# Kernel tuning notes

Measured on AMD Instinct MI355X. Metric: run time of the kernel, lower is better.

The kernel has to match this reference:

```python
import jax, jax.numpy as jnp
import numpy as np

BS, SEQ, D, H = 2, 2048, 1024, 16
HD = D // H  # head_dim = 64


def setup_inputs() -> dict:
    key = jax.random.key(0)
    kx, kw = jax.random.split(key)
    x = jax.random.normal(kx, (BS, SEQ, D), dtype=jnp.float32)
    # qkv Linear: weight [3D, D] (xavier_normal), bias zeros
    std = float(np.sqrt(2.0 / (D + 3 * D)))
    W_qkv = jax.random.normal(kw, (3 * D, D), dtype=jnp.float32) * std
    b_qkv = jnp.zeros((3 * D,), dtype=jnp.float32)
    return {"x": x, "W_qkv": W_qkv, "b_qkv": b_qkv}


def reference(x, W_qkv, b_qkv):
    bs, seq_len, embed_dim = x.shape
    # fused QKV projection: [bs, seq, 3D]
    qkv = x @ W_qkv.T + b_qkv
    qkv = qkv.reshape(bs, seq_len, 3, H, HD)
    qkv = jnp.transpose(qkv, (2, 0, 3, 1, 4))  # [3, bs, H, seq, HD]
    Q, K, V = qkv[0], qkv[1], qkv[2]
    # past_kv is None -> total_len == seq_len, past_len == 0
    scores = jnp.einsum("bhqd,bhkd->bhqk", Q, K) / jnp.sqrt(jnp.float32(HD))
    # causal mask: True above diagonal -> -inf
    mask = jnp.triu(jnp.ones((seq_len, seq_len), dtype=bool), k=1)
    scores = jnp.where(mask[None, None, :, :], -jnp.inf, scores)
    probs = jax.nn.softmax(scores, axis=-1)
    # attn_dropout = 0.0 (eval) -> identity
    out = jnp.einsum("bhqk,bhkd->bhqd", probs, V)
    out = jnp.transpose(out, (0, 2, 1, 3)).reshape(bs, seq_len, embed_dim)
    return (out, (K, V))
```

## Files before the change

kernel.cpp:

```cpp
#include <hip/hip_runtime.h>

typedef __bf16 bf16_t;
typedef __bf16 bf16x8 __attribute__((ext_vector_type(8)));
typedef float f32x4 __attribute__((ext_vector_type(4)));
typedef unsigned long long u64;

__device__ __forceinline__ unsigned short bfbits(float f) {
  unsigned u = __float_as_uint(f);
  u += 0x7fffu + ((u >> 16) & 1u);
  return (unsigned short)(u >> 16);
}
__device__ __forceinline__ bf16_t f2bf(float f) {
  unsigned short s = bfbits(f);
  union { unsigned short s; bf16_t b; } cv; cv.s = s; return cv.b;
}

__device__ __forceinline__ void gl16(const void* g, void* l) {
  __builtin_amdgcn_global_load_lds(
      (const __attribute__((address_space(1))) void*)g,
      (__attribute__((address_space(3))) void*)l,
      16, 0, 0);
}

__global__ __launch_bounds__(256) void cvt_kernel(const float* __restrict__ x,
                                                  const float* __restrict__ Wf,
                                                  bf16_t* __restrict__ xb,
                                                  bf16_t* __restrict__ wb) {
  const int i = blockIdx.x * 256 + threadIdx.x;
  const float* src; bf16_t* dst; int j;
  if (i < 524288) { j = i; src = x; dst = xb; }
  else            { j = i - 524288; src = Wf; dst = wb; }
  const float4* s = (const float4*)src + (size_t)j * 2;
  float4 a = s[0], b = s[1];
  bf16x8 o;
  o[0] = f2bf(a.x); o[1] = f2bf(a.y); o[2] = f2bf(a.z); o[3] = f2bf(a.w);
  o[4] = f2bf(b.x); o[5] = f2bf(b.y); o[6] = f2bf(b.z); o[7] = f2bf(b.w);
  const int row = j >> 7, jr = j & 127;
  const int dstc = (row << 7) + (jr & ~3) + ((jr & 3) ^ ((row >> 1) & 3));
  *((bf16x8*)dst + dstc) = o;
}

#define GEMM_K 1024
__global__ __launch_bounds__(256) void qkv_gemm(
    const bf16_t* __restrict__ A,
    const bf16_t* __restrict__ B,
    const float* __restrict__ bias,
    float* __restrict__ Ko, float* __restrict__ Vo,
    bf16_t* __restrict__ Qb, bf16_t* __restrict__ Kb,
    bf16_t* __restrict__ Vt,
    int* __restrict__ qcnt)
{
  if (blockIdx.x == 0 && threadIdx.x == 0) *qcnt = 0;
  __shared__ bf16_t lsA[3][4096];
  __shared__ bf16_t lsB[3][4096];
  const int tid = threadIdx.x;
  const int lane = tid & 63;
  const int ln = lane & 15, qd = lane >> 4;
  const int wid = tid >> 6;
  const int wm = wid & 1, wn = wid >> 1;
  const int xcd = blockIdx.x & 7;
  const int j = blockIdx.x >> 3;
  const int bn = xcd * 3 + (j % 3);
  const int bm = j / 3;
  const int m0 = bm * 128, n0 = bn * 128;
  const int qs = qd ^ ((ln >> 1) & 3);

  f32x4 acc[4][4] = {};

  const int c0 = tid, c1 = tid + 256;
  const bf16_t* ga0 = A + (size_t)(m0 + (c0 >> 2)) * GEMM_K + (c0 & 3) * 8;
  const bf16_t* ga1 = A + (size_t)(m0 + (c1 >> 2)) * GEMM_K + (c1 & 3) * 8;
  const bf16_t* gb0 = B + (size_t)(n0 + (c0 >> 2)) * GEMM_K + (c0 & 3) * 8;
  const bf16_t* gb1 = B + (size_t)(n0 + (c1 >> 2)) * GEMM_K + (c1 & 3) * 8;

#define STAGE(t, slot)                                   \
  do {                                                   \
    const int ko_ = (t) * 32;                            \
    gl16(ga0 + ko_, &lsA[(slot)][c0 * 8]);               \
    gl16(ga1 + ko_, &lsA[(slot)][c1 * 8]);               \
    gl16(gb0 + ko_, &lsB[(slot)][c0 * 8]);               \
    gl16(gb1 + ko_, &lsB[(slot)][c1 * 8]);               \
  } while (0)

#define COMPUTE(slot)                                                          \
  do {                                                                         \
    bf16x8 af[4], bf[4];                                                       \
    _Pragma("unroll")                                                          \
    for (int mi = 0; mi < 4; ++mi)                                             \
      af[mi] = *(const bf16x8*)&lsA[(slot)][(wm * 64 + mi * 16 + ln) * 32 + qs * 8]; \
    _Pragma("unroll")                                                          \
    for (int ni = 0; ni < 4; ++ni)                                             \
      bf[ni] = *(const bf16x8*)&lsB[(slot)][(wn * 64 + ni * 16 + ln) * 32 + qs * 8]; \
    _Pragma("unroll")                                                          \
    for (int mi = 0; mi < 4; ++mi)                                             \
      _Pragma("unroll")                                                        \
      for (int ni = 0; ni < 4; ++ni)                                           \
        acc[mi][ni] = __builtin_amdgcn_mfma_f32_16x16x32_bf16(af[mi], bf[ni], acc[mi][ni], 0, 0, 0); \
  } while (0)

#define WAITBAR(n)                                        \
  do {                                                    \
    asm volatile("s_waitcnt vmcnt(" #n ")" ::: "memory"); \
    __builtin_amdgcn_s_barrier();                         \
  } while (0)

  STAGE(0, 0);
  STAGE(1, 1);
#pragma unroll
  for (int t = 0; t < 30; ++t) {
    WAITBAR(4);
    STAGE(t + 2, (t + 2) % 3);
    COMPUTE(t % 3);
  }
  WAITBAR(4); COMPUTE(0);
  WAITBAR(0); COMPUTE(1);

#undef STAGE
#undef COMPUTE
#undef WAITBAR

  const int sec = n0 >> 10;
#pragma unroll
  for (int mi = 0; mi < 4; ++mi) {
#pragma unroll
    for (int ni = 0; ni < 4; ++ni) {
      const int colg = n0 + wn * 64 + ni * 16 + ln;
      const float bv = bias[colg];
      const int cc = colg & 1023, h = cc >> 6, hd = cc & 63;
      if (sec == 2) {
        unsigned u[4];
#pragma unroll
        for (int r = 0; r < 4; ++r) {
          const int mg = m0 + wm * 64 + mi * 16 + qd * 4 + r;
          const int b = mg >> 11, s = mg & 2047;
          const float val = acc[mi][ni][r] + bv;
          Vo[((size_t)((b * 16 + h) * 2048 + s)) * 64 + hd] = val;
          u[r] = __float_as_uint(val);
        }
        const int mg0 = m0 + wm * 64 + mi * 16 + qd * 4;
        const int b0 = mg0 >> 11, s0 = mg0 & 2047;
        const unsigned lo = (u[1] & 0xFFFF0000u) | (u[0] >> 16);
        const unsigned hi = (u[3] & 0xFFFF0000u) | (u[2] >> 16);
        const size_t vb = (size_t)(b0 * 16 + h) * 131072 + (size_t)(s0 >> 6) * 4096 +
                          (size_t)hd * 64 + ((((s0 >> 3) & 7) ^ (hd & 7)) << 3) + (s0 & 7);
        *(u64*)&Vt[vb] = ((u64)hi << 32) | lo;
      } else {
#pragma unroll
        for (int r = 0; r < 4; ++r) {
          const int mg = m0 + wm * 64 + mi * 16 + qd * 4 + r;
          const int b = mg >> 11, s = mg & 2047;
          const float val = acc[mi][ni][r] + bv;
          const int bhi = b * 16 + h;
          const size_t sidx = (size_t)bhi * 131072 + (size_t)(s >> 6) * 4096 +
                              (size_t)(s & 63) * 64 + (((hd >> 3) ^ (s & 7)) << 3) + (hd & 7);
          if (sec == 0) {
            Qb[sidx] = f2bf(val * 0.18033688f);
          } else {
            Ko[((size_t)(bhi * 2048 + s)) * 64 + hd] = val;
            Kb[sidx] = f2bf(val);
          }
        }
      }
    }
  }
}

__global__ __launch_bounds__(512, 4) void attn_kernel(
    const bf16_t* __restrict__ Qb,
    const bf16_t* __restrict__ Kb,
    const bf16_t* __restrict__ Vt,
    float* __restrict__ Out,
    int* __restrict__ qcnt)
{
  __shared__ bf16_t lk[8192];
  __shared__ bf16_t lv[8192];
  __shared__ bf16_t lp[8192];
  __shared__ int task_sh;
  const int tid = threadIdx.x;
  const int lane = tid & 63, ln = lane & 15, qd = lane >> 4;
  const int w = tid >> 6;
  const int l7 = ln & 7;

  for (;;) {
    __syncthreads();
    if (tid == 0) task_sh = atomicAdd(qcnt, 1);
    __syncthreads();
    const int task = task_sh;
    if (task >= 512) break;
    const int it = (task < 256) ? (15 - (task >> 5)) : ((task - 256) >> 5);
    const int bh = task & 31;
    const int b = bh >> 4, h = bh & 15;

    const bf16_t* qbase = Qb + (size_t)bh * 131072 + (size_t)it * 8192;
    const bf16_t* kbase = Kb + (size_t)bh * 131072;
    const bf16_t* vbase = Vt + (size_t)bh * 131072;

#pragma unroll
    for (int i = 0; i < 2; ++i) {
      const int cc = tid + i * 512;
      gl16(kbase + cc * 8, &lk[cc * 8]);
      gl16(vbase + cc * 8, &lv[cc * 8]);
    }

    bf16x8 afq[2];
    {
      const int row = w * 16 + ln;
#pragma unroll
      for (int kk = 0; kk < 2; ++kk)
        afq[kk] = *(const bf16x8*)(qbase + (row >> 6) * 4096 + (row & 63) * 64 +
                                   (((kk * 4 + qd) ^ l7) << 3));
    }
    __syncthreads();

    f32x4 oc[4] = {};
    float lsum = 0.f;
    const int qg = it * 128 + w * 16 + ln;
    const int q = w * 16 + ln;

    for (int st = 0; st <= it; ++st) {
      if (st > 0) {
        __syncthreads();
#pragma unroll
        for (int i = 0; i < 2; ++i) {
          const int cc = tid + i * 512;
          gl16(kbase + (size_t)st * 8192 + cc * 8, &lk[cc * 8]);
          gl16(vbase + (size_t)st * 8192 + cc * 8, &lv[cc * 8]);
        }
        __syncthreads();
      }
      const bool diag = (st == it);

#pragma unroll
      for (int h2 = 0; h2 < 2; ++h2) {
        const int lofs = h2 * 4096;
        f32x4 sa[4] = {};
#pragma unroll
        for (int kk = 0; kk < 2; ++kk) {
          bf16x8 ak[4];
#pragma unroll
          for (int ki = 0; ki < 4; ++ki)
            ak[ki] = *(const bf16x8*)&lk[lofs + (ki * 16 + ln) * 64 + (((kk * 4 + qd) ^ l7) << 3)];
#pragma unroll
          for (int ki = 0; ki < 4; ++ki)
            sa[ki] = __builtin_amdgcn_mfma_f32_16x16x32_bf16(ak[ki], afq[kk], sa[ki], 0, 0, 0);
        }

#pragma unroll
        for (int ki = 0; ki < 4; ++ki) {
          const int kb0 = (st * 2 + h2) * 64 + ki * 16 + qd * 4;
          float p0 = __builtin_amdgcn_exp2f(sa[ki][0]);
          float p1 = __builtin_amdgcn_exp2f(sa[ki][1]);
          float p2 = __builtin_amdgcn_exp2f(sa[ki][2]);
          float p3 = __builtin_amdgcn_exp2f(sa[ki][3]);
          if (diag) {
            if (kb0 + 0 > qg) p0 = 0.f;
            if (kb0 + 1 > qg) p1 = 0.f;
            if (kb0 + 2 > qg) p2 = 0.f;
            if (kb0 + 3 > qg) p3 = 0.f;
          }
          lsum += (p0 + p1) + (p2 + p3);
          const unsigned lo = (__float_as_uint(p1) & 0xFFFF0000u) | (__float_as_uint(p0) >> 16);
          const unsigned hi = (__float_as_uint(p3) & 0xFFFF0000u) | (__float_as_uint(p2) >> 16);
          const int g = (ki * 2 + (qd >> 1)) ^ l7;
          *(u64*)&lp[q * 64 + g * 8 + (qd & 1) * 4] = ((u64)hi << 32) | lo;
        }

#pragma unroll
        for (int kk = 0; kk < 2; ++kk) {
          bf16x8 afp, bfv[4];
          afp = *(const bf16x8*)&lp[q * 64 + (((kk * 4 + qd) ^ l7) << 3)];
#pragma unroll
          for (int ni = 0; ni < 4; ++ni)
            bfv[ni] = *(const bf16x8*)&lv[lofs + (ni * 16 + ln) * 64 + (((kk * 4 + qd) ^ l7) << 3)];
#pragma unroll
          for (int ni = 0; ni < 4; ++ni)
            oc[ni] = __builtin_amdgcn_mfma_f32_16x16x32_bf16(afp, bfv[ni], oc[ni], 0, 0, 0);
        }
      }
    }

    float ls = lsum;
    ls += __shfl_xor(ls, 16);
    ls += __shfl_xor(ls, 32);
#pragma unroll
    for (int r = 0; r < 4; ++r) {
      const float lval = __shfl(ls, qd * 4 + r);
      const float inv = 1.0f / lval;
      const int rowq = it * 128 + w * 16 + qd * 4 + r;
#pragma unroll
      for (int ni = 0; ni < 4; ++ni) {
        const int colh = ni * 16 + ln;
        Out[(size_t)(b * 2048 + rowq) * 1024 + h * 64 + colh] = oc[ni][r] * inv;
      }
    }
  }
}

extern "C" void kernel_launch(void* const* d_in, const int* in_sizes, int n_in,
                              void* d_out, int out_size, void* d_ws, size_t ws_size,
                              hipStream_t stream) {
  const float* x = (const float*)d_in[0];
  const float* W = (const float*)d_in[1];
  const float* bq = (const float*)d_in[2];
  float* out = (float*)d_out;
  float* Ko = out + 4194304;
  float* Vo = out + 8388608;
  char* ws = (char*)d_ws;
  bf16_t* xb = (bf16_t*)ws;
  bf16_t* wb = (bf16_t*)(ws + 8388608);
  bf16_t* Qb = (bf16_t*)(ws + 14680064);
  bf16_t* Kb = (bf16_t*)(ws + 23068672);
  bf16_t* Vt = (bf16_t*)(ws + 31457280);
  int*    qcnt = (int*)(ws + 39845888);

  hipLaunchKernelGGL(cvt_kernel, dim3(3584), dim3(256), 0, stream, x, W, xb, wb);
  hipLaunchKernelGGL(qkv_gemm, dim3(768), dim3(256), 0, stream, xb, wb, bq, Ko, Vo, Qb, Kb, Vt, qcnt);
  hipLaunchKernelGGL(attn_kernel, dim3(512), dim3(512), 0, stream, Qb, Kb, Vt, out, qcnt);
}
```

Measured before the change: 161.5 us.

## Double-buffer K/V tiles in LDS and skip fully masked diagonal subtile

Splits the K/V shared-memory staging into two 64-key slots and prefetches the next tile with async global-to-LDS loads while computing the current one. The two __syncthreads per 128-key block become a vmcnt wait plus barrier per 64-key tile. Waves whose query rows all lie before the final 64-key tile now skip it, since it is entirely masked. The risk is that the single wait-and-barrier must also cover the reuse of the P scratch buffer and the overwrite of the slot just read.

```diff
diff --git a/kernel.cpp b/kernel.cpp
--- a/kernel.cpp
+++ b/kernel.cpp
@@ -172,8 +172,8 @@
     float* __restrict__ Out,
     int* __restrict__ qcnt)
 {
-  __shared__ bf16_t lk[8192];
-  __shared__ bf16_t lv[8192];
+  __shared__ bf16_t lk[2][4096];
+  __shared__ bf16_t lv[2][4096];
   __shared__ bf16_t lp[8192];
   __shared__ int task_sh;
   const int tid = threadIdx.x;
@@ -195,13 +195,73 @@
     const bf16_t* kbase = Kb + (size_t)bh * 131072;
     const bf16_t* vbase = Vt + (size_t)bh * 131072;
 
-#pragma unroll
-    for (int i = 0; i < 2; ++i) {
-      const int cc = tid + i * 512;
-      gl16(kbase + cc * 8, &lk[cc * 8]);
-      gl16(vbase + cc * 8, &lv[cc * 8]);
-    }
-
+    f32x4 oc[4] = {};
+    float lsum = 0.f;
+    const int qg = it * 128 + w * 16 + ln;
+    const int q = w * 16 + ln;
+    const int nt = 2 * (it + 1);
+
+#define STG(t, slot)                                              \
+    do {                                                          \
+      gl16(kbase + (size_t)(t) * 4096 + tid * 8, &lk[(slot)][tid * 8]); \
+      gl16(vbase + (size_t)(t) * 4096 + tid * 8, &lv[(slot)][tid * 8]); \
+    } while (0)
+
+#define CTILE(kt, slot)                                                        \
+    do {                                                                       \
+      if (!((kt) == 2 * it + 1 && w < 4)) {                                    \
+        const bool diag = ((kt) >= 2 * it);                                    \
+        f32x4 sa[4] = {};                                                      \
+        _Pragma("unroll")                                                      \
+        for (int kk = 0; kk < 2; ++kk) {                                       \
+          bf16x8 ak[4];                                                        \
+          _Pragma("unroll")                                                    \
+          for (int ki = 0; ki < 4; ++ki)                                       \
+            ak[ki] = *(const bf16x8*)&lk[(slot)][(ki * 16 + ln) * 64 + (((kk * 4 + qd) ^ l7) << 3)]; \
+          _Pragma("unroll")                                                    \
+          for (int ki = 0; ki < 4; ++ki)                                       \
+            sa[ki] = __builtin_amdgcn_mfma_f32_16x16x32_bf16(ak[ki], afq[kk], sa[ki], 0, 0, 0); \
+        }                                                                      \
+        _Pragma("unroll")                                                      \
+        for (int ki = 0; ki < 4; ++ki) {                                       \
+          const int kb0 = (kt) * 64 + ki * 16 + qd * 4;                        \
+          float p0 = __builtin_amdgcn_exp2f(sa[ki][0]);                        \
+          float p1 = __builtin_amdgcn_exp2f(sa[ki][1]);                        \
+          float p2 = __builtin_amdgcn_exp2f(sa[ki][2]);                        \
+          float p3 = __builtin_amdgcn_exp2f(sa[ki][3]);                        \
+          if (diag) {                                                          \
+            if (kb0 + 0 > qg) p0 = 0.f;                                        \
+            if (kb0 + 1 > qg) p1 = 0.f;                                        \
+            if (kb0 + 2 > qg) p2 = 0.f;                                        \
+            if (kb0 + 3 > qg) p3 = 0.f;                                        \
+          }                                                                    \
+          lsum += (p0 + p1) + (p2 + p3);                                       \
+          const unsigned lo = (__float_as_uint(p1) & 0xFFFF0000u) | (__float_as_uint(p0) >> 16); \
+          const unsigned hi = (__float_as_uint(p3) & 0xFFFF0000u) | (__float_as_uint(p2) >> 16); \
+          const int g = (ki * 2 + (qd >> 1)) ^ l7;                             \
+          *(u64*)&lp[q * 64 + g * 8 + (qd & 1) * 4] = ((u64)hi << 32) | lo;    \
+        }                                                                      \
+        _Pragma("unroll")                                                      \
+        for (int kk = 0; kk < 2; ++kk) {                                       \
+          bf16x8 afp, bfv[4];                                                  \
+          afp = *(const bf16x8*)&lp[q * 64 + (((kk * 4 + qd) ^ l7) << 3)];     \
+          _Pragma("unroll")                                                    \
+          for (int ni = 0; ni < 4; ++ni)                                       \
+            bfv[ni] = *(const bf16x8*)&lv[(slot)][(ni * 16 + ln) * 64 + (((kk * 4 + qd) ^ l7) << 3)]; \
+          _Pragma("unroll")                                                    \
+          for (int ni = 0; ni < 4; ++ni)                                       \
+            oc[ni] = __builtin_amdgcn_mfma_f32_16x16x32_bf16(afp, bfv[ni], oc[ni], 0, 0, 0); \
+        }                                                                      \
+      }                                                                        \
+    } while (0)
+
+#define WB0                                               \
+    do {                                                  \
+      asm volatile("s_waitcnt vmcnt(0)" ::: "memory");    \
+      __builtin_amdgcn_s_barrier();                       \
+    } while (0)
+
+    STG(0, 0);
     bf16x8 afq[2];
     {
       const int row = w * 16 + ln;
@@ -210,74 +270,20 @@
         afq[kk] = *(const bf16x8*)(qbase + (row >> 6) * 4096 + (row & 63) * 64 +
                                    (((kk * 4 + qd) ^ l7) << 3));
     }
-    __syncthreads();
-
-    f32x4 oc[4] = {};
-    float lsum = 0.f;
-    const int qg = it * 128 + w * 16 + ln;
-    const int q = w * 16 + ln;
-
-    for (int st = 0; st <= it; ++st) {
-      if (st > 0) {
-        __syncthreads();
-#pragma unroll
-        for (int i = 0; i < 2; ++i) {
-          const int cc = tid + i * 512;
-          gl16(kbase + (size_t)st * 8192 + cc * 8, &lk[cc * 8]);
-          gl16(vbase + (size_t)st * 8192 + cc * 8, &lv[cc * 8]);
-        }
-        __syncthreads();
-      }
-      const bool diag = (st == it);
-
-#pragma unroll
-      for (int h2 = 0; h2 < 2; ++h2) {
-        const int lofs = h2 * 4096;
-        f32x4 sa[4] = {};
-#pragma unroll
-        for (int kk = 0; kk < 2; ++kk) {
-          bf16x8 ak[4];
-#pragma unroll
-          for (int ki = 0; ki < 4; ++ki)
-            ak[ki] = *(const bf16x8*)&lk[lofs + (ki * 16 + ln) * 64 + (((kk * 4 + qd) ^ l7) << 3)];
-#pragma unroll
-          for (int ki = 0; ki < 4; ++ki)
-            sa[ki] = __builtin_amdgcn_mfma_f32_16x16x32_bf16(ak[ki], afq[kk], sa[ki], 0, 0, 0);
-        }
-
-#pragma unroll
-        for (int ki = 0; ki < 4; ++ki) {
-          const int kb0 = (st * 2 + h2) * 64 + ki * 16 + qd * 4;
-          float p0 = __builtin_amdgcn_exp2f(sa[ki][0]);
-          float p1 = __builtin_amdgcn_exp2f(sa[ki][1]);
-          float p2 = __builtin_amdgcn_exp2f(sa[ki][2]);
-          float p3 = __builtin_amdgcn_exp2f(sa[ki][3]);
-          if (diag) {
-            if (kb0 + 0 > qg) p0 = 0.f;
-            if (kb0 + 1 > qg) p1 = 0.f;
-            if (kb0 + 2 > qg) p2 = 0.f;
-            if (kb0 + 3 > qg) p3 = 0.f;
-          }
-          lsum += (p0 + p1) + (p2 + p3);
-          const unsigned lo = (__float_as_uint(p1) & 0xFFFF0000u) | (__float_as_uint(p0) >> 16);
-          const unsigned hi = (__float_as_uint(p3) & 0xFFFF0000u) | (__float_as_uint(p2) >> 16);
-          const int g = (ki * 2 + (qd >> 1)) ^ l7;
-          *(u64*)&lp[q * 64 + g * 8 + (qd & 1) * 4] = ((u64)hi << 32) | lo;
-        }
-
-#pragma unroll
-        for (int kk = 0; kk < 2; ++kk) {
-          bf16x8 afp, bfv[4];
-          afp = *(const bf16x8*)&lp[q * 64 + (((kk * 4 + qd) ^ l7) << 3)];
-#pragma unroll
-          for (int ni = 0; ni < 4; ++ni)
-            bfv[ni] = *(const bf16x8*)&lv[lofs + (ni * 16 + ln) * 64 + (((kk * 4 + qd) ^ l7) << 3)];
-#pragma unroll
-          for (int ni = 0; ni < 4; ++ni)
-            oc[ni] = __builtin_amdgcn_mfma_f32_16x16x32_bf16(afp, bfv[ni], oc[ni], 0, 0, 0);
-        }
-      }
+    WB0;
+
+    for (int s = 0; s < nt; s += 2) {
+      STG(s + 1, 1);
+      CTILE(s, 0);
+      WB0;
+      if (s + 2 < nt) STG(s + 2, 0);
+      CTILE(s + 1, 1);
+      WB0;
     }
+
+#undef STG
+#undef CTILE
+#undef WB0
 
     float ls = lsum;
     ls += __shfl_xor(ls, 16);
```

Result: slower. 165.9 us (+2.7%).
